# Optimization experiments

Hardware: AMD Instinct MI355X
Metric: run time of the kernel (lower is better)

The kernel has to match this reference:

```python
import jax, jax.numpy as jnp
import numpy as np

T, D, H, E = 8192, 1024, 512, 8
BLK = 32  # MXFP8 scaling block size along the contraction dim


def setup_inputs() -> dict:
    key = jax.random.key(0)
    k1, k2, k3, k4 = jax.random.split(key, 4)
    # qdata: values representable-ish in e4m3 (we use small normal floats)
    output_e4m3 = jax.random.normal(k1, (T, D), dtype=jnp.float32)
    # e8m0 scales are powers of two, one per 32-element block along dim
    output_scales_e8m0 = jnp.exp2(
        jax.random.randint(k2, (T, D // BLK), -2, 3).astype(jnp.float32)
    )
    # uniform token distribution across experts (tokens are expert-contiguous)
    num_tokens_per_expert = jnp.full((E,), T // E, dtype=jnp.int32)
    expert_padded_offsets = jnp.zeros((E,), dtype=jnp.int32)  # unused by forward body
    w13 = jax.random.normal(k3, (E, 2 * H, D), dtype=jnp.float32) * 0.02
    w2 = jax.random.normal(k4, (E, D, H), dtype=jnp.float32) * 0.02
    return {
        "output_e4m3": output_e4m3,
        "output_scales_e8m0": output_scales_e8m0,
        "num_tokens_per_expert": num_tokens_per_expert,
        "expert_padded_offsets": expert_padded_offsets,
        "w13": w13,
        "w2": w2,
    }


def reference(output_e4m3, output_scales_e8m0, num_tokens_per_expert,
              expert_padded_offsets, w13, w2):
    # Dequantize MXFP8: qdata * per-block e8m0 scale, blocks of 32 along dim.
    scales = jnp.repeat(output_scales_e8m0, BLK, axis=-1)  # [T, D]
    x = output_e4m3 * scales  # [T, D] high-precision reference activations
    # Grouped GEMM 1: tokens are expert-contiguous with uniform group sizes,
    # so the ragged grouped matmul reduces to a batched einsum per expert.
    tpe = T // E
    xg = x.reshape(E, tpe, D)                       # [E, tpe, D]
    h13 = jnp.einsum("etd,ehd->eth", xg, w13)       # [E, tpe, 2H]
    h1, h3 = h13[..., :H], h13[..., H:]
    h = jax.nn.silu(h1) * h3                        # fused SiLU-gate
    # Grouped GEMM 2
    out = jnp.einsum("eth,edh->etd", h, w2)         # [E, tpe, D]
    return out.reshape(T, D)
```

## Files before the change

kernel.cpp:

```cpp
#include <hip/hip_runtime.h>
#include <hip/hip_bf16.h>

#define T_TOK 8192
#define DDIM  1024
#define HDIM  512
#define NE    8
#define TPE   (T_TOK / NE)

typedef __attribute__((ext_vector_type(4))) float floatx4;
typedef __attribute__((ext_vector_type(8))) short bf16x8;

__device__ __forceinline__ unsigned short f2bf(float f) {
    union { float f; unsigned int u; } v;
    v.f = f;
    unsigned int u = v.u;
    unsigned int r = u + 0x7FFFu + ((u >> 16) & 1u);
    return (unsigned short)(r >> 16);
}

__device__ __forceinline__ unsigned int cvt_pk_bf16(float lo, float hi) {
    unsigned int r;
    asm("v_cvt_pk_bf16_f32 %0, %1, %2" : "=v"(r) : "v"(lo), "v"(hi));
    return r;
}

__device__ __forceinline__ void gld_lds16(const void* g, void* l) {
    __builtin_amdgcn_global_load_lds(
        (const __attribute__((address_space(1))) unsigned int*)g,
        (__attribute__((address_space(3))) unsigned int*)l, 16, 0, 0);
}

__global__ __launch_bounds__(256)
void convert_kernel(const float* __restrict__ X, const float* __restrict__ S,
                    const float* __restrict__ W13,
                    unsigned short* __restrict__ Xb,
                    unsigned short* __restrict__ W13b)
{
    const int NTX  = (T_TOK * DDIM) / 4;
    const int NT13 = (NE * 2 * HDIM * DDIM) / 4;
    const int stride = gridDim.x * blockDim.x;
    for (int i = blockIdx.x * blockDim.x + threadIdx.x; i < NTX + NT13; i += stride) {
        float4 v;
        ushort4* dst;
        if (i < NTX) {
            int row = i >> 8;
            int c4  = i & 255;
            v = reinterpret_cast<const float4*>(X)[i];
            float sc = S[row * (DDIM / 32) + (c4 >> 3)];
            v.x *= sc; v.y *= sc; v.z *= sc; v.w *= sc;
            dst = (ushort4*)Xb + i;
        } else {
            int j = i - NTX;
            v = reinterpret_cast<const float4*>(W13)[j];
            dst = (ushort4*)W13b + j;
        }
        ushort4 b;
        b.x = f2bf(v.x); b.y = f2bf(v.y); b.z = f2bf(v.z); b.w = f2bf(v.w);
        *dst = b;
    }
}

__device__ __forceinline__ int xcd_swizzle_512(int raw) {
    return (raw & 7) * 64 + (raw >> 3);
}


__global__ __launch_bounds__(256, 2)
void gemm1_silu_kernel(const unsigned short* __restrict__ Xb,
                       const unsigned short* __restrict__ W13b,
                       __hip_bfloat16* __restrict__ Hout)
{
    const int bid = xcd_swizzle_512(blockIdx.x);
    const int e  = bid >> 6;
    const int mt = (bid >> 3) & 7;
    const int nt = bid & 7;
    const int tok0 = e * TPE + mt * 128;
    const unsigned short* __restrict__ We = W13b + (size_t)e * (2 * HDIM) * DDIM;

    __shared__ __hip_bfloat16 sA[2][128][64];
    __shared__ __hip_bfloat16 sB[2][128][64];

    const int tid  = threadIdx.x;
    const int lane = tid & 63;
    const int wave = tid >> 6;
    const int wr = wave >> 1;
    const int wc = wave & 1;
    const int lr = lane & 15;
    const int sw0 = ((lane >> 4) ^ (lane & 7));

    floatx4 acc1[4][2] = {};
    floatx4 acc3[4][2] = {};

    const int srow0 = (tid >> 3);
    const int dcol  = (tid & 7) * 8;
    const int gcol  = ((tid & 7) ^ (srow0 & 7)) * 8;

    auto STAGE = [&](int kk, int buf) {
        const int k0 = kk * 64;
        #pragma unroll
        for (int j = 0; j < 4; ++j) {
            int row = srow0 + j * 32;
            gld_lds16(&Xb[(size_t)(tok0 + row) * DDIM + k0 + gcol],
                      &sA[buf][row][dcol]);
            int wrow = (j < 2) ? (nt * 64 + row)
                               : (HDIM + nt * 64 + (row - 64));
            gld_lds16(&We[(size_t)wrow * DDIM + k0 + gcol],
                      &sB[buf][row][dcol]);
        }
    };
    auto COMPUTE = [&](int buf) {
        #pragma unroll
        for (int ks = 0; ks < 2; ++ks) {
            const int rc = (sw0 ^ (ks << 2)) << 3;
            bf16x8 a[4], b1[2], b3[2];
            #pragma unroll
            for (int m = 0; m < 4; ++m)
                a[m] = *reinterpret_cast<const bf16x8*>(&sA[buf][wr * 64 + m * 16 + lr][rc]);
            #pragma unroll
            for (int n = 0; n < 2; ++n) {
                b1[n] = *reinterpret_cast<const bf16x8*>(&sB[buf][wc * 32 + n * 16 + lr][rc]);
                b3[n] = *reinterpret_cast<const bf16x8*>(&sB[buf][64 + wc * 32 + n * 16 + lr][rc]);
            }
            #pragma unroll
            for (int m = 0; m < 4; ++m)
                #pragma unroll
                for (int n = 0; n < 2; ++n) {
                    acc1[m][n] = __builtin_amdgcn_mfma_f32_16x16x32_bf16(a[m], b1[n], acc1[m][n], 0, 0, 0);
                    acc3[m][n] = __builtin_amdgcn_mfma_f32_16x16x32_bf16(a[m], b3[n], acc3[m][n], 0, 0, 0);
                }
        }
    };

    STAGE(0, 0);
    for (int kk = 0; kk < DDIM / 64 - 1; ++kk) {
        STAGE(kk + 1, (kk + 1) & 1);
        asm volatile("s_waitcnt vmcnt(8)" ::: "memory");
        __builtin_amdgcn_sched_barrier(0);
        __builtin_amdgcn_s_barrier();
        COMPUTE(kk & 1);
        __builtin_amdgcn_s_barrier();
    }
    asm volatile("s_waitcnt vmcnt(0)" ::: "memory");
    __builtin_amdgcn_sched_barrier(0);
    __builtin_amdgcn_s_barrier();
    COMPUTE(1);

    const int hcol0 = nt * 64 + wc * 32;
    #pragma unroll
    for (int m = 0; m < 4; ++m) {
        #pragma unroll
        for (int n = 0; n < 2; ++n) {
            #pragma unroll
            for (int i = 0; i < 4; ++i) {
                int row = tok0 + wr * 64 + m * 16 + (lane >> 4) * 4 + i;
                int col = hcol0 + n * 16 + (lane & 15);
                float h1 = acc1[m][n][i];
                float h3 = acc3[m][n][i];
                float sig = 1.0f / (1.0f + __expf(-h1));
                Hout[(size_t)row * HDIM + col] = __float2bfloat16(h1 * sig * h3);
            }
        }
    }
}

__global__ __launch_bounds__(256, 2)
void gemm2_kernel(const __hip_bfloat16* __restrict__ Hin,
                  const float* __restrict__ W2,
                  float* __restrict__ Out)
{
    const int bid = xcd_swizzle_512(blockIdx.x);
    const int e  = bid >> 6;
    const int nt = (bid >> 3) & 7;
    const int mt = bid & 7;
    const int tok0 = e * TPE + mt * 128;
    const float* __restrict__ We = W2 + (size_t)e * DDIM * HDIM;

    __shared__ __hip_bfloat16 sA[2][128][64];
    __shared__ __hip_bfloat16 sB[2][128][64];

    const int tid  = threadIdx.x;
    const int lane = tid & 63;
    const int wave = tid >> 6;
    const int wr = wave >> 1;
    const int wc = wave & 1;
    const int lr = lane & 15;
    const int sw0 = ((lane >> 4) ^ (lane & 7));

    floatx4 acc[4][4] = {};

    const int srow0 = (tid >> 3);
    const int c8    = (tid & 7) * 8;
    const int dcol  = (tid & 7) * 8;
    const int swcol = ((tid & 7) ^ (srow0 & 7)) * 8;

    float4 rB[8];

    auto LOADB = [&](int kk) {
        const int k0 = kk * 64;
        #pragma unroll
        for (int j = 0; j < 4; ++j) {
            int row = srow0 + j * 32;
            const float* p = &We[(size_t)(nt * 128 + row) * HDIM + k0 + c8];
            rB[2*j]   = *reinterpret_cast<const float4*>(p);
            rB[2*j+1] = *reinterpret_cast<const float4*>(p + 4);
        }
    };
    auto STAGEA = [&](int kk, int buf) {
        const int k0 = kk * 64;
        #pragma unroll
        for (int j = 0; j < 4; ++j) {
            int row = srow0 + j * 32;
            gld_lds16(&Hin[(size_t)(tok0 + row) * HDIM + k0 + swcol],
                      &sA[buf][row][dcol]);
        }
    };
    auto WRITEB = [&](int buf) {
        #pragma unroll
        for (int j = 0; j < 4; ++j) {
            int row = srow0 + j * 32;
            uint4 w;
            w.x = cvt_pk_bf16(rB[2*j].x,   rB[2*j].y);
            w.y = cvt_pk_bf16(rB[2*j].z,   rB[2*j].w);
            w.z = cvt_pk_bf16(rB[2*j+1].x, rB[2*j+1].y);
            w.w = cvt_pk_bf16(rB[2*j+1].z, rB[2*j+1].w);
            *reinterpret_cast<uint4*>(&sB[buf][row][swcol]) = w;
        }
    };
    auto COMPUTE = [&](int buf) {
        #pragma unroll
        for (int ks = 0; ks < 2; ++ks) {
            const int rc = (sw0 ^ (ks << 2)) << 3;
            bf16x8 a[4], b[4];
            #pragma unroll
            for (int m = 0; m < 4; ++m)
                a[m] = *reinterpret_cast<const bf16x8*>(&sA[buf][wr * 64 + m * 16 + lr][rc]);
            #pragma unroll
            for (int n = 0; n < 4; ++n)
                b[n] = *reinterpret_cast<const bf16x8*>(&sB[buf][wc * 64 + n * 16 + lr][rc]);
            #pragma unroll
            for (int m = 0; m < 4; ++m)
                #pragma unroll
                for (int n = 0; n < 4; ++n)
                    acc[m][n] = __builtin_amdgcn_mfma_f32_16x16x32_bf16(a[m], b[n], acc[m][n], 0, 0, 0);
        }
    };

    LOADB(0);
    __builtin_amdgcn_sched_barrier(0);
    STAGEA(0, 0);
    __builtin_amdgcn_sched_barrier(0);
    for (int kk = 0; kk < HDIM / 64 - 1; ++kk) {
        const int buf = kk & 1;
        asm volatile("s_waitcnt vmcnt(4)" ::: "memory");
        __builtin_amdgcn_sched_barrier(0);
        WRITEB(buf);
        __builtin_amdgcn_sched_barrier(0);
        LOADB(kk + 1);
        __builtin_amdgcn_sched_barrier(0);
        STAGEA(kk + 1, buf ^ 1);
        __builtin_amdgcn_sched_barrier(0);
        asm volatile("s_waitcnt vmcnt(12) lgkmcnt(0)" ::: "memory");
        __builtin_amdgcn_sched_barrier(0);
        __builtin_amdgcn_s_barrier();
        COMPUTE(buf);
        __builtin_amdgcn_s_barrier();
    }
    asm volatile("s_waitcnt vmcnt(4)" ::: "memory");
    __builtin_amdgcn_sched_barrier(0);
    WRITEB(1);
    asm volatile("s_waitcnt vmcnt(0) lgkmcnt(0)" ::: "memory");
    __builtin_amdgcn_sched_barrier(0);
    __builtin_amdgcn_s_barrier();
    COMPUTE(1);

    const int dcol0 = nt * 128 + wc * 64;
    #pragma unroll
    for (int m = 0; m < 4; ++m) {
        #pragma unroll
        for (int n = 0; n < 4; ++n) {
            #pragma unroll
            for (int i = 0; i < 4; ++i) {
                int row = tok0 + wr * 64 + m * 16 + (lane >> 4) * 4 + i;
                int col = dcol0 + n * 16 + (lane & 15);
                Out[(size_t)row * DDIM + col] = acc[m][n][i];
            }
        }
    }
}

extern "C" void kernel_launch(void* const* d_in, const int* in_sizes, int n_in,
                              void* d_out, int out_size, void* d_ws, size_t ws_size,
                              hipStream_t stream) {
    const float* X   = (const float*)d_in[0];
    const float* S   = (const float*)d_in[1];
    const float* W13 = (const float*)d_in[4];
    const float* W2  = (const float*)d_in[5];
    float* Out = (float*)d_out;

    unsigned short* W13b = (unsigned short*)d_ws;
    __hip_bfloat16* Hb   = (__hip_bfloat16*)(W13b + (size_t)NE * 2 * HDIM * DDIM);
    unsigned short* Xb   = (unsigned short*)d_out;

    convert_kernel<<<2048, 256, 0, stream>>>(X, S, W13, Xb, W13b);
    gemm1_silu_kernel<<<NE * 8 * 8, 256, 0, stream>>>(Xb, W13b, Hb);
    gemm2_kernel<<<NE * 8 * 8, 256, 0, stream>>>(Hb, W2, Out);
}
```

Before: 57.59 us.

## Enlarge gemm1 tile to 256 rows with 8 waves; software-pipeline gemm2 weight loads

```diff
diff --git a/kernel.cpp b/kernel.cpp
--- a/kernel.cpp
+++ b/kernel.cpp
@@ -9,6 +9,8 @@
 
 typedef __attribute__((ext_vector_type(4))) float floatx4;
 typedef __attribute__((ext_vector_type(8))) short bf16x8;
+
+#define SBAR() __builtin_amdgcn_sched_barrier(0)
 
 __device__ __forceinline__ unsigned short f2bf(float f) {
     union { float f; unsigned int u; } v;
@@ -63,21 +65,24 @@
 __device__ __forceinline__ int xcd_swizzle_512(int raw) {
     return (raw & 7) * 64 + (raw >> 3);
 }
-
-
-__global__ __launch_bounds__(256, 2)
+__device__ __forceinline__ int xcd_swizzle_256(int raw) {
+    return (raw & 7) * 32 + (raw >> 3);
+}
+
+
+__global__ __launch_bounds__(512, 2)
 void gemm1_silu_kernel(const unsigned short* __restrict__ Xb,
                        const unsigned short* __restrict__ W13b,
                        __hip_bfloat16* __restrict__ Hout)
 {
-    const int bid = xcd_swizzle_512(blockIdx.x);
-    const int e  = bid >> 6;
-    const int mt = (bid >> 3) & 7;
+    const int bid = xcd_swizzle_256(blockIdx.x);
+    const int e  = bid >> 5;
+    const int mt = (bid >> 3) & 3;
     const int nt = bid & 7;
-    const int tok0 = e * TPE + mt * 128;
+    const int tok0 = e * TPE + mt * 256;
     const unsigned short* __restrict__ We = W13b + (size_t)e * (2 * HDIM) * DDIM;
 
-    __shared__ __hip_bfloat16 sA[2][128][64];
+    __shared__ __hip_bfloat16 sA[2][256][64];
     __shared__ __hip_bfloat16 sB[2][128][64];
 
     const int tid  = threadIdx.x;
@@ -91,22 +96,25 @@
     floatx4 acc1[4][2] = {};
     floatx4 acc3[4][2] = {};
 
-    const int srow0 = (tid >> 3);
-    const int dcol  = (tid & 7) * 8;
-    const int gcol  = ((tid & 7) ^ (srow0 & 7)) * 8;
+    const int srowA = tid >> 3;
+    const int dcolA = (tid & 7) * 8;
+    const int gcolA = ((tid & 7) ^ (srowA & 7)) * 8;
+    const int srowB = tid >> 3;
+    const int dcolB = (tid & 7) * 8;
+    const int gcolB = ((tid & 7) ^ (srowB & 7)) * 8;
 
     auto STAGE = [&](int kk, int buf) {
         const int k0 = kk * 64;
         #pragma unroll
         for (int j = 0; j < 4; ++j) {
-            int row = srow0 + j * 32;
-            gld_lds16(&Xb[(size_t)(tok0 + row) * DDIM + k0 + gcol],
-                      &sA[buf][row][dcol]);
-            int wrow = (j < 2) ? (nt * 64 + row)
-                               : (HDIM + nt * 64 + (row - 64));
-            gld_lds16(&We[(size_t)wrow * DDIM + k0 + gcol],
-                      &sB[buf][row][dcol]);
-        }
+            int row = srowA + j * 64;
+            gld_lds16(&Xb[(size_t)(tok0 + row) * DDIM + k0 + gcolA],
+                      &sA[buf][row][dcolA]);
+        }
+        gld_lds16(&We[(size_t)(nt * 64 + srowB) * DDIM + k0 + gcolB],
+                  &sB[buf][srowB][dcolB]);
+        gld_lds16(&We[(size_t)(HDIM + nt * 64 + srowB) * DDIM + k0 + gcolB],
+                  &sB[buf][64 + srowB][dcolB]);
     };
     auto COMPUTE = [&](int buf) {
         #pragma unroll
@@ -134,14 +142,14 @@
     STAGE(0, 0);
     for (int kk = 0; kk < DDIM / 64 - 1; ++kk) {
         STAGE(kk + 1, (kk + 1) & 1);
-        asm volatile("s_waitcnt vmcnt(8)" ::: "memory");
-        __builtin_amdgcn_sched_barrier(0);
+        asm volatile("s_waitcnt vmcnt(6)" ::: "memory");
+        SBAR();
         __builtin_amdgcn_s_barrier();
         COMPUTE(kk & 1);
         __builtin_amdgcn_s_barrier();
     }
     asm volatile("s_waitcnt vmcnt(0)" ::: "memory");
-    __builtin_amdgcn_sched_barrier(0);
+    SBAR();
     __builtin_amdgcn_s_barrier();
     COMPUTE(1);
 
@@ -193,9 +201,9 @@
     const int dcol  = (tid & 7) * 8;
     const int swcol = ((tid & 7) ^ (srow0 & 7)) * 8;
 
-    float4 rB[8];
-
-    auto LOADB = [&](int kk) {
+    float4 rB0[8], rB1[8];
+
+    auto LOADB = [&](int kk, float4* rB) {
         const int k0 = kk * 64;
         #pragma unroll
         for (int j = 0; j < 4; ++j) {
@@ -214,7 +222,7 @@
                       &sA[buf][row][dcol]);
         }
     };
-    auto WRITEB = [&](int buf) {
+    auto WRITEB = [&](int buf, const float4* rB) {
         #pragma unroll
         for (int j = 0; j < 4; ++j) {
             int row = srow0 + j * 32;
@@ -245,31 +253,44 @@
         }
     };
 
-    LOADB(0);
-    __builtin_amdgcn_sched_barrier(0);
-    STAGEA(0, 0);
-    __builtin_amdgcn_sched_barrier(0);
-    for (int kk = 0; kk < HDIM / 64 - 1; ++kk) {
-        const int buf = kk & 1;
-        asm volatile("s_waitcnt vmcnt(4)" ::: "memory");
-        __builtin_amdgcn_sched_barrier(0);
-        WRITEB(buf);
-        __builtin_amdgcn_sched_barrier(0);
-        LOADB(kk + 1);
-        __builtin_amdgcn_sched_barrier(0);
-        STAGEA(kk + 1, buf ^ 1);
-        __builtin_amdgcn_sched_barrier(0);
-        asm volatile("s_waitcnt vmcnt(12) lgkmcnt(0)" ::: "memory");
-        __builtin_amdgcn_sched_barrier(0);
+    LOADB(0, rB0);  SBAR();
+    STAGEA(0, 0);   SBAR();
+    LOADB(1, rB1);  SBAR();
+    asm volatile("s_waitcnt vmcnt(12)" ::: "memory");
+    SBAR();
+    WRITEB(0, rB0); SBAR();
+    asm volatile("s_waitcnt vmcnt(8) lgkmcnt(0)" ::: "memory");
+    SBAR();
+    __builtin_amdgcn_s_barrier();
+
+    for (int t = 0; t < HDIM / 64 - 2; t += 2) {
+        STAGEA(t + 1, 1);   SBAR();
+        LOADB(t + 2, rB0);  SBAR();
+        COMPUTE(0);
+        asm volatile("s_waitcnt vmcnt(12)" ::: "memory");
+        SBAR();
+        WRITEB(1, rB1);     SBAR();
+        asm volatile("s_waitcnt vmcnt(8) lgkmcnt(0)" ::: "memory");
+        SBAR();
         __builtin_amdgcn_s_barrier();
-        COMPUTE(buf);
+        STAGEA(t + 2, 0);   SBAR();
+        LOADB(t + 3, rB1);  SBAR();
+        COMPUTE(1);
+        asm volatile("s_waitcnt vmcnt(12)" ::: "memory");
+        SBAR();
+        WRITEB(0, rB0);     SBAR();
+        asm volatile("s_waitcnt vmcnt(8) lgkmcnt(0)" ::: "memory");
+        SBAR();
         __builtin_amdgcn_s_barrier();
     }
+
+    STAGEA(7, 1);   SBAR();
+    COMPUTE(0);
     asm volatile("s_waitcnt vmcnt(4)" ::: "memory");
-    __builtin_amdgcn_sched_barrier(0);
-    WRITEB(1);
+    SBAR();
+    WRITEB(1, rB1); SBAR();
     asm volatile("s_waitcnt vmcnt(0) lgkmcnt(0)" ::: "memory");
-    __builtin_amdgcn_sched_barrier(0);
+    SBAR();
     __builtin_amdgcn_s_barrier();
     COMPUTE(1);
 
@@ -302,6 +323,6 @@
     unsigned short* Xb   = (unsigned short*)d_out;
 
     convert_kernel<<<2048, 256, 0, stream>>>(X, S, W13, Xb, W13b);
-    gemm1_silu_kernel<<<NE * 8 * 8, 256, 0, stream>>>(Xb, W13b, Hb);
+    gemm1_silu_kernel<<<NE * 4 * 8, 512, 0, stream>>>(Xb, W13b, Hb);
     gemm2_kernel<<<NE * 8 * 8, 256, 0, stream>>>(Hb, W2, Out);
 }
```

Result: slower. 59.64 us (+3.5%).
